# Kernel tuning notes

Measured on AMD Instinct MI355X. Metric: run time of the kernel, lower is better.

The kernel has to match this reference:

```python
import jax, jax.numpy as jnp
import numpy as np

IN_SIZE = 1024
HIDDEN = 1024
BATCH = 4096


def _linear_params(key, out_dim, in_dim):
    # torch nn.Linear init: U(-1/sqrt(in_dim), 1/sqrt(in_dim)) for W and b
    k1, k2 = jax.random.split(key)
    bound = 1.0 / np.sqrt(in_dim)
    W = jax.random.uniform(k1, (out_dim, in_dim), jnp.float32, -bound, bound)
    b = jax.random.uniform(k2, (out_dim,), jnp.float32, -bound, bound)
    return W, b


def setup_inputs() -> dict:
    key = jax.random.key(0)
    keys = jax.random.split(key, 11)
    x = jax.random.normal(keys[0], (BATCH, IN_SIZE), jnp.float32)
    hidden = jax.random.normal(keys[1], (BATCH, HIDDEN), jnp.float32)
    cell = jax.random.normal(keys[2], (BATCH, HIDDEN), jnp.float32)
    names = ['xf', 'xi', 'xo', 'xc', 'hf', 'hi', 'ho', 'hc']
    inp = {'x': x, 'hidden': hidden, 'cell': cell}
    for n, k in zip(names, keys[3:]):
        in_dim = IN_SIZE if n[0] == 'x' else HIDDEN
        W, b = _linear_params(k, HIDDEN, in_dim)
        inp['W_' + n] = W
        inp['b_' + n] = b
    return inp


def reference(x, hidden, cell,
              W_xf, b_xf, W_xi, b_xi, W_xo, b_xo, W_xc, b_xc,
              W_hf, b_hf, W_hi, b_hi, W_ho, b_ho, W_hc, b_hc):
    # gates: sigmoid/tanh over (x-linear + h-linear) pairs
    f = jax.nn.sigmoid(x @ W_xf.T + b_xf + hidden @ W_hf.T + b_hf)
    i = jax.nn.sigmoid(x @ W_xi.T + b_xi + hidden @ W_hi.T + b_hi)
    o = jax.nn.sigmoid(x @ W_xo.T + b_xo + hidden @ W_ho.T + b_ho)
    c = jnp.tanh(x @ W_xc.T + b_xc + hidden @ W_hc.T + b_hc)
    updated_cell = f * cell + i * c
    updated_hidden = o * jnp.tanh(updated_cell)
    return updated_hidden, updated_cell
```

## Files before the change

### kernel.cpp

```cpp
#include <hip/hip_runtime.h>
#include <hip/hip_bf16.h>

#define BATCH 4096
#define NH    1024
#define KCAT  2048
#define NJ    4096
#define NT    (KCAT / 64)

typedef __bf16 bf16x8 __attribute__((ext_vector_type(8)));
typedef float  f32x4  __attribute__((ext_vector_type(4)));
typedef unsigned short u16x8 __attribute__((ext_vector_type(8)));

struct WPtrs { const float* wx[4]; const float* wh[4]; };
struct BPtrs { const float* bx[4]; const float* bh[4]; };

__device__ __forceinline__ unsigned short f2b(float f) {
  union { float f; unsigned u; } v; v.f = f;
  return (unsigned short)((v.u + 0x7fffu + ((v.u >> 16) & 1u)) >> 16);
}

__device__ __forceinline__ void gload_lds16(const void* g, void* l) {
  __builtin_amdgcn_global_load_lds(
      (const __attribute__((address_space(1))) unsigned int*)g,
      (__attribute__((address_space(3))) unsigned int*)l, 16, 0, 0);
}

__device__ __forceinline__ float sigmoid_f(float x) {
  x = fminf(fmaxf(x, -30.f), 30.f);
  return 1.f / (1.f + __expf(-x));
}
__device__ __forceinline__ float tanh_f(float x) {
  x = fminf(fmaxf(x, -15.f), 15.f);
  float e = __expf(2.f * x);
  return (e - 1.f) / (e + 1.f);
}


__global__ __launch_bounds__(256) void pack_a(const float* __restrict__ x,
                                              const float* __restrict__ h,
                                              __hip_bfloat16* __restrict__ Acat) {
  int t = blockIdx.x * 256 + threadIdx.x;
  int base = t * 8;
  int row = base >> 11;
  int k   = base & 2047;
  const float* src = (k < 1024) ? (x + (size_t)row * 1024 + k)
                                : (h + (size_t)row * 1024 + (k - 1024));
  float4 v0 = ((const float4*)src)[0];
  float4 v1 = ((const float4*)src)[1];
  u16x8 o;
  o[0]=f2b(v0.x); o[1]=f2b(v0.y); o[2]=f2b(v0.z); o[3]=f2b(v0.w);
  o[4]=f2b(v1.x); o[5]=f2b(v1.y); o[6]=f2b(v1.z); o[7]=f2b(v1.w);
  *(u16x8*)((unsigned short*)Acat + base) = o;
}

__global__ __launch_bounds__(256) void pack_b(WPtrs W, __hip_bfloat16* __restrict__ Bcat) {
  int t = blockIdx.x * 256 + threadIdx.x;
  int base = t * 8;
  int j = base >> 11;
  int k = base & 2047;
  int n = ((j >> 6) << 4) + (j & 15);
  int g = (j >> 4) & 3;
  const float* src = (k < 1024) ? (W.wx[g] + (size_t)n * 1024 + k)
                                : (W.wh[g] + (size_t)n * 1024 + (k - 1024));
  float4 v0 = ((const float4*)src)[0];
  float4 v1 = ((const float4*)src)[1];
  u16x8 o;
  o[0]=f2b(v0.x); o[1]=f2b(v0.y); o[2]=f2b(v0.z); o[3]=f2b(v0.w);
  o[4]=f2b(v1.x); o[5]=f2b(v1.y); o[6]=f2b(v1.z); o[7]=f2b(v1.w);
  *(u16x8*)((unsigned short*)Bcat + base) = o;
}

__global__ __launch_bounds__(256) void pack_bias(BPtrs B, float* __restrict__ biasc) {
  int i = blockIdx.x * 256 + threadIdx.x;
  int g = i >> 10, n = i & 1023;
  biasc[i] = B.bx[g][n] + B.bh[g][n];
}

#define STAGE_HALF(Mg, MOFF, T, H, B)                                           \
  {                                                                             \
    _Pragma("unroll")                                                           \
    for (int i_ = 0; i_ < 2; ++i_) {                                            \
      const unsigned short* src_ =                                              \
          (Mg) + (size_t)((H) * 128 + i_ * 64 + strow) * KCAT + (T) * 64 +      \
          stchnk * 8;                                                           \
      unsigned short* dst_ =                                                    \
          &smem[(B) * 32768 + (MOFF) + (H) * 8192 + i_ * 4096 + w * 512];       \
      gload_lds16(src_, dst_);                                                  \
    }                                                                           \
  }

__global__ __launch_bounds__(512, 2) void lstm_gemm8(
    const unsigned short* __restrict__ Acat,
    const unsigned short* __restrict__ Bcat,
    const float* __restrict__ biasc,
    const float* __restrict__ cell,
    float* __restrict__ outH, float* __restrict__ outC) {
  __shared__ unsigned short smem[65536];

  const int tid  = threadIdx.x;
  const int w    = tid >> 6;
  const int lane = tid & 63;
  const int wr   = w >> 2;
  const int wc   = w & 3;
  const int lr   = lane & 15;
  const int cb0  = ((lane >> 4) & 3) * 16;
  const int sx   = (lr & 7) << 4;

  const int bid = blockIdx.x;
  const int s   = (bid & 7) * 32 + (bid >> 3);
  const int bx  = s & 15;
  const int by  = s >> 4;

  const unsigned short* Ag = Acat + (size_t)(by * 256) * KCAT;
  const unsigned short* Bg = Bcat + (size_t)(bx * 256) * KCAT;

  const int strow  = w * 8 + (lane >> 3);
  const int stchnk = (lane & 7) ^ ((lane >> 3) & 7);

  const int arow0 = (wr * 128 + lr) * 128;
  const int brow0 = 32768 + (wc * 64 + lr) * 128;
  const int colb0 = cb0 ^ sx;
  const int colb1 = (64 + cb0) ^ sx;
  const char* smc = (const char*)smem;

  f32x4 acc[8][4] = {};

  STAGE_HALF(Ag, 0,     0, 0, 0);
  STAGE_HALF(Ag, 0,     0, 1, 0);
  STAGE_HALF(Bg, 16384, 0, 0, 0);
  STAGE_HALF(Bg, 16384, 0, 1, 0);
  STAGE_HALF(Bg, 16384, 1, 0, 1);
  STAGE_HALF(Bg, 16384, 1, 1, 1);
  asm volatile("s_waitcnt vmcnt(4)" ::: "memory");
  __builtin_amdgcn_sched_barrier(0);
  __builtin_amdgcn_s_barrier();

  for (int t = 0; t < NT; ++t) {
    const int cur  = t & 1;
    const int curo = cur * 65536;
    bf16x8 bfr[4][2];
#pragma unroll
    for (int p = 0; p < 4; ++p) {
      bf16x8 af[2][2];
#pragma unroll
      for (int mi = 0; mi < 2; ++mi) {
        af[mi][0] = *(const bf16x8*)(smc + curo + arow0 + (2*p+mi)*2048 + colb0);
        af[mi][1] = *(const bf16x8*)(smc + curo + arow0 + (2*p+mi)*2048 + colb1);
      }
      if (p == 0) {
#pragma unroll
        for (int n = 0; n < 4; ++n) {
          bfr[n][0] = *(const bf16x8*)(smc + curo + brow0 + n*2048 + colb0);
          bfr[n][1] = *(const bf16x8*)(smc + curo + brow0 + n*2048 + colb1);
        }
      }
      if (p == 0 && t + 1 < NT) STAGE_HALF(Ag, 0,     t + 1, 0, cur ^ 1);
      if (p == 1 && t + 1 < NT) STAGE_HALF(Ag, 0,     t + 1, 1, cur ^ 1);
      if (p == 2 && t + 2 < NT) STAGE_HALF(Bg, 16384, t + 2, 0, cur);
      if (p == 3 && t + 2 < NT) STAGE_HALF(Bg, 16384, t + 2, 1, cur);
      __builtin_amdgcn_sched_barrier(0);
      __builtin_amdgcn_s_barrier();
      asm volatile("s_waitcnt lgkmcnt(0)" ::: "memory");
      __builtin_amdgcn_sched_barrier(0);
      __builtin_amdgcn_s_setprio(1);
#pragma unroll
      for (int mi = 0; mi < 2; ++mi)
#pragma unroll
        for (int n = 0; n < 4; ++n) {
          acc[2*p+mi][n] = __builtin_amdgcn_mfma_f32_16x16x32_bf16(
              af[mi][0], bfr[n][0], acc[2*p+mi][n], 0, 0, 0);
          acc[2*p+mi][n] = __builtin_amdgcn_mfma_f32_16x16x32_bf16(
              af[mi][1], bfr[n][1], acc[2*p+mi][n], 0, 0, 0);
        }
      __builtin_amdgcn_s_setprio(0);
      if (p == 3) {
        if (t < NT - 2) {
          asm volatile("s_waitcnt vmcnt(4)" ::: "memory");
        } else if (t == NT - 2) {
          asm volatile("s_waitcnt vmcnt(0)" ::: "memory");
        }
        __builtin_amdgcn_sched_barrier(0);
      }
      __builtin_amdgcn_s_barrier();
    }
  }

  const int n_out = (bx * 4 + wc) * 16 + lr;
  const float bfv = biasc[n_out];
  const float biv = biasc[1024 + n_out];
  const float bov = biasc[2048 + n_out];
  const float bcv = biasc[3072 + n_out];
  const int q0 = (lane >> 4) * 4;

#pragma unroll
  for (int m = 0; m < 8; ++m) {
    int row0 = by * 256 + wr * 128 + m * 16 + q0;
#pragma unroll
    for (int q = 0; q < 4; ++q) {
      int row = row0 + q;
      float pf = acc[m][0][q] + bfv;
      float pi = acc[m][1][q] + biv;
      float po = acc[m][2][q] + bov;
      float pc = acc[m][3][q] + bcv;
      float fg = sigmoid_f(pf);
      float ig = sigmoid_f(pi);
      float og = sigmoid_f(po);
      float cg = tanh_f(pc);
      float cold = cell[(size_t)row * NH + n_out];
      float cn = fg * cold + ig * cg;
      float hn = og * tanh_f(cn);
      outH[(size_t)row * NH + n_out] = hn;
      outC[(size_t)row * NH + n_out] = cn;
    }
  }
}

extern "C" void kernel_launch(void* const* d_in, const int* in_sizes, int n_in,
                              void* d_out, int out_size, void* d_ws, size_t ws_size,
                              hipStream_t stream) {
  const float* x    = (const float*)d_in[0];
  const float* h    = (const float*)d_in[1];
  const float* cell = (const float*)d_in[2];
  WPtrs wp; BPtrs bp;
  for (int g = 0; g < 4; ++g) {
    wp.wx[g] = (const float*)d_in[3 + 2 * g];
    bp.bx[g] = (const float*)d_in[4 + 2 * g];
    wp.wh[g] = (const float*)d_in[11 + 2 * g];
    bp.bh[g] = (const float*)d_in[12 + 2 * g];
  }

  char* ws = (char*)d_ws;
  __hip_bfloat16* Acat = (__hip_bfloat16*)ws;
  __hip_bfloat16* Bcat = (__hip_bfloat16*)(ws + (size_t)BATCH * KCAT * 2);
  float* biasc = (float*)(ws + (size_t)BATCH * KCAT * 2 + (size_t)NJ * KCAT * 2);

  float* outH = (float*)d_out;
  float* outC = outH + (size_t)BATCH * NH;

  pack_a<<<BATCH * KCAT / 8 / 256, 256, 0, stream>>>(x, h, Acat);
  pack_b<<<NJ * KCAT / 8 / 256, 256, 0, stream>>>(wp, Bcat);
  pack_bias<<<NJ / 1024 * 4, 256, 0, stream>>>(bp, biasc);

  lstm_gemm8<<<256, 512, 0, stream>>>((const unsigned short*)Acat,
                                      (const unsigned short*)Bcat,
                                      biasc, cell, outH, outC);
}
```

Before: 91.13 us.

## Merge pack kernels and re-slice A prefetch into per-wave slices across phases

The three packing kernels are merged into one launch that dispatches on block index, removing two kernel launches. In the GEMM main loop, A-tile staging is split into four per-wave 32-row slices spread across the four phases, so A for tile t+2 is prefetched earlier alongside B. The vmcnt/lgkmcnt waits are adjusted to match. The bias loads are hoisted ahead of the main loop. The finer-grained slicing is meant to spread global-to-LDS traffic more evenly and deepen prefetch, but it makes the buffer reuse and wait counts more delicate to get right.

```diff
diff --git a/kernel.cpp b/kernel.cpp
--- a/kernel.cpp
+++ b/kernel.cpp
@@ -35,58 +35,71 @@
   return (e - 1.f) / (e + 1.f);
 }
 
-
-__global__ __launch_bounds__(256) void pack_a(const float* __restrict__ x,
-                                              const float* __restrict__ h,
-                                              __hip_bfloat16* __restrict__ Acat) {
-  int t = blockIdx.x * 256 + threadIdx.x;
-  int base = t * 8;
-  int row = base >> 11;
-  int k   = base & 2047;
-  const float* src = (k < 1024) ? (x + (size_t)row * 1024 + k)
-                                : (h + (size_t)row * 1024 + (k - 1024));
-  float4 v0 = ((const float4*)src)[0];
-  float4 v1 = ((const float4*)src)[1];
-  u16x8 o;
-  o[0]=f2b(v0.x); o[1]=f2b(v0.y); o[2]=f2b(v0.z); o[3]=f2b(v0.w);
-  o[4]=f2b(v1.x); o[5]=f2b(v1.y); o[6]=f2b(v1.z); o[7]=f2b(v1.w);
-  *(u16x8*)((unsigned short*)Acat + base) = o;
-}
-
-__global__ __launch_bounds__(256) void pack_b(WPtrs W, __hip_bfloat16* __restrict__ Bcat) {
-  int t = blockIdx.x * 256 + threadIdx.x;
-  int base = t * 8;
-  int j = base >> 11;
-  int k = base & 2047;
-  int n = ((j >> 6) << 4) + (j & 15);
-  int g = (j >> 4) & 3;
-  const float* src = (k < 1024) ? (W.wx[g] + (size_t)n * 1024 + k)
-                                : (W.wh[g] + (size_t)n * 1024 + (k - 1024));
-  float4 v0 = ((const float4*)src)[0];
-  float4 v1 = ((const float4*)src)[1];
-  u16x8 o;
-  o[0]=f2b(v0.x); o[1]=f2b(v0.y); o[2]=f2b(v0.z); o[3]=f2b(v0.w);
-  o[4]=f2b(v1.x); o[5]=f2b(v1.y); o[6]=f2b(v1.z); o[7]=f2b(v1.w);
-  *(u16x8*)((unsigned short*)Bcat + base) = o;
-}
-
-__global__ __launch_bounds__(256) void pack_bias(BPtrs B, float* __restrict__ biasc) {
-  int i = blockIdx.x * 256 + threadIdx.x;
-  int g = i >> 10, n = i & 1023;
-  biasc[i] = B.bx[g][n] + B.bh[g][n];
-}
-
-#define STAGE_HALF(Mg, MOFF, T, H, B)                                           \
+__global__ __launch_bounds__(256) void pack_all(
+    const float* __restrict__ x, const float* __restrict__ h,
+    WPtrs W, BPtrs B,
+    __hip_bfloat16* __restrict__ Acat, __hip_bfloat16* __restrict__ Bcat,
+    float* __restrict__ biasc) {
+  int bid = blockIdx.x;
+  if (bid < 4096) {
+    int t = bid * 256 + threadIdx.x;
+    int base = t * 8;
+    int row = base >> 11;
+    int k   = base & 2047;
+    const float* src = (k < 1024) ? (x + (size_t)row * 1024 + k)
+                                  : (h + (size_t)row * 1024 + (k - 1024));
+    float4 v0 = ((const float4*)src)[0];
+    float4 v1 = ((const float4*)src)[1];
+    u16x8 o;
+    o[0]=f2b(v0.x); o[1]=f2b(v0.y); o[2]=f2b(v0.z); o[3]=f2b(v0.w);
+    o[4]=f2b(v1.x); o[5]=f2b(v1.y); o[6]=f2b(v1.z); o[7]=f2b(v1.w);
+    *(u16x8*)((unsigned short*)Acat + base) = o;
+  } else if (bid < 8192) {
+    int t = (bid - 4096) * 256 + threadIdx.x;
+    int base = t * 8;
+    int j = base >> 11;
+    int k = base & 2047;
+    int n = ((j >> 6) << 4) + (j & 15);
+    int g = (j >> 4) & 3;
+    const float* src = (k < 1024) ? (W.wx[g] + (size_t)n * 1024 + k)
+                                  : (W.wh[g] + (size_t)n * 1024 + (k - 1024));
+    float4 v0 = ((const float4*)src)[0];
+    float4 v1 = ((const float4*)src)[1];
+    u16x8 o;
+    o[0]=f2b(v0.x); o[1]=f2b(v0.y); o[2]=f2b(v0.z); o[3]=f2b(v0.w);
+    o[4]=f2b(v1.x); o[5]=f2b(v1.y); o[6]=f2b(v1.z); o[7]=f2b(v1.w);
+    *(u16x8*)((unsigned short*)Bcat + base) = o;
+  } else {
+    int i = (bid - 8192) * 256 + threadIdx.x;
+    int g = i >> 10, n = i & 1023;
+    biasc[i] = B.bx[g][n] + B.bh[g][n];
+  }
+}
+
+
+#define STAGE_A_HALF(T, H)                                                      \
   {                                                                             \
     _Pragma("unroll")                                                           \
     for (int i_ = 0; i_ < 2; ++i_) {                                            \
-      const unsigned short* src_ =                                              \
-          (Mg) + (size_t)((H) * 128 + i_ * 64 + strow) * KCAT + (T) * 64 +      \
-          stchnk * 8;                                                           \
-      unsigned short* dst_ =                                                    \
-          &smem[(B) * 32768 + (MOFF) + (H) * 8192 + i_ * 4096 + w * 512];       \
-      gload_lds16(src_, dst_);                                                  \
+      gload_lds16(Ag + (size_t)((H)*128 + i_*64 + strow) * KCAT + (T)*64 +      \
+                      stchnk * 8,                                               \
+                  &smem[((T)&1)*32768 + (H)*8192 + i_*4096 + w*512]);           \
     }                                                                           \
+  }
+#define STAGE_B_HALF(T, H)                                                      \
+  {                                                                             \
+    _Pragma("unroll")                                                           \
+    for (int i_ = 0; i_ < 2; ++i_) {                                            \
+      gload_lds16(Bg + (size_t)((H)*128 + i_*64 + strow) * KCAT + (T)*64 +      \
+                      stchnk * 8,                                               \
+                  &smem[((T)&1)*32768 + 16384 + (H)*8192 + i_*4096 + w*512]);   \
+    }                                                                           \
+  }
+#define STAGE_A_SLICE(T, S)                                                     \
+  {                                                                             \
+    gload_lds16(Ag + (size_t)(arbw + (S)*32 + (lane >> 3)) * KCAT + (T)*64 +    \
+                    stchnk * 8,                                                 \
+                &smem[((T)&1)*32768 + (arbw + (S)*32) * 64]);                   \
   }
 
 __global__ __launch_bounds__(512, 2) void lstm_gemm8(
@@ -116,6 +129,7 @@
 
   const int strow  = w * 8 + (lane >> 3);
   const int stchnk = (lane & 7) ^ ((lane >> 3) & 7);
+  const int arbw   = (w >> 2) * 128 + (w & 3) * 8;
 
   const int arow0 = (wr * 128 + lr) * 128;
   const int brow0 = 32768 + (wc * 64 + lr) * 128;
@@ -123,15 +137,24 @@
   const int colb1 = (64 + cb0) ^ sx;
   const char* smc = (const char*)smem;
 
+  const int n_out = (bx * 4 + wc) * 16 + lr;
+  const float bfv = biasc[n_out];
+  const float biv = biasc[1024 + n_out];
+  const float bov = biasc[2048 + n_out];
+  const float bcv = biasc[3072 + n_out];
+
   f32x4 acc[8][4] = {};
 
-  STAGE_HALF(Ag, 0,     0, 0, 0);
-  STAGE_HALF(Ag, 0,     0, 1, 0);
-  STAGE_HALF(Bg, 16384, 0, 0, 0);
-  STAGE_HALF(Bg, 16384, 0, 1, 0);
-  STAGE_HALF(Bg, 16384, 1, 0, 1);
-  STAGE_HALF(Bg, 16384, 1, 1, 1);
-  asm volatile("s_waitcnt vmcnt(4)" ::: "memory");
+  STAGE_A_HALF(0, 0);
+  STAGE_A_HALF(0, 1);
+  STAGE_B_HALF(0, 0);
+  STAGE_B_HALF(0, 1);
+  STAGE_A_SLICE(1, 0);
+  STAGE_A_SLICE(1, 1);
+  STAGE_A_SLICE(1, 2);
+  STAGE_B_HALF(1, 0);
+  STAGE_B_HALF(1, 1);
+  asm volatile("s_waitcnt vmcnt(7)" ::: "memory");
   __builtin_amdgcn_sched_barrier(0);
   __builtin_amdgcn_s_barrier();
 
@@ -154,10 +177,11 @@
           bfr[n][1] = *(const bf16x8*)(smc + curo + brow0 + n*2048 + colb1);
         }
       }
-      if (p == 0 && t + 1 < NT) STAGE_HALF(Ag, 0,     t + 1, 0, cur ^ 1);
-      if (p == 1 && t + 1 < NT) STAGE_HALF(Ag, 0,     t + 1, 1, cur ^ 1);
-      if (p == 2 && t + 2 < NT) STAGE_HALF(Bg, 16384, t + 2, 0, cur);
-      if (p == 3 && t + 2 < NT) STAGE_HALF(Bg, 16384, t + 2, 1, cur);
+      if (p == 0 && t + 1 < NT) STAGE_A_SLICE(t + 1, 3);
+      if (p == 1 && t + 2 < NT) { STAGE_A_SLICE(t + 2, 0); STAGE_B_HALF(t + 2, 0); }
+      if (p == 2 && t + 2 < NT) { STAGE_A_SLICE(t + 2, 1); STAGE_B_HALF(t + 2, 1); }
+      if (p == 3 && t + 2 < NT) STAGE_A_SLICE(t + 2, 2);
+      if (p == 0) asm volatile("s_waitcnt lgkmcnt(8)" ::: "memory");
       __builtin_amdgcn_sched_barrier(0);
       __builtin_amdgcn_s_barrier();
       asm volatile("s_waitcnt lgkmcnt(0)" ::: "memory");
@@ -175,7 +199,7 @@
       __builtin_amdgcn_s_setprio(0);
       if (p == 3) {
         if (t < NT - 2) {
-          asm volatile("s_waitcnt vmcnt(4)" ::: "memory");
+          asm volatile("s_waitcnt vmcnt(7)" ::: "memory");
         } else if (t == NT - 2) {
           asm volatile("s_waitcnt vmcnt(0)" ::: "memory");
         }
@@ -185,13 +209,7 @@
     }
   }
 
-  const int n_out = (bx * 4 + wc) * 16 + lr;
-  const float bfv = biasc[n_out];
-  const float biv = biasc[1024 + n_out];
-  const float bov = biasc[2048 + n_out];
-  const float bcv = biasc[3072 + n_out];
   const int q0 = (lane >> 4) * 4;
-
 #pragma unroll
   for (int m = 0; m < 8; ++m) {
     int row0 = by * 256 + wr * 128 + m * 16 + q0;
@@ -237,9 +255,7 @@
   float* outH = (float*)d_out;
   float* outC = outH + (size_t)BATCH * NH;
 
-  pack_a<<<BATCH * KCAT / 8 / 256, 256, 0, stream>>>(x, h, Acat);
-  pack_b<<<NJ * KCAT / 8 / 256, 256, 0, stream>>>(wp, Bcat);
-  pack_bias<<<NJ / 1024 * 4, 256, 0, stream>>>(bp, biasc);
+  pack_all<<<8208, 256, 0, stream>>>(x, h, wp, bp, Acat, Bcat, biasc);
 
   lstm_gemm8<<<256, 512, 0, stream>>>((const unsigned short*)Acat,
                                       (const unsigned short*)Bcat,
```

Measured after the change: 88.01 us. -3.4%, faster.
